# Kernel tuning notes

Hardware: AMD Instinct MI355X
Metric: run time of the kernel (lower is better)

The kernel has to match this reference:

```python
import jax, jax.numpy as jnp
import numpy as np

EPS = 1e-5
DIM, QK, PDIM, SR = 256, 64, 128, 2
B, H, W = 16, 64, 64
SCALE = QK ** (-0.5)


def _conv(x, w, stride, pad, groups=1):
    return jax.lax.conv_general_dilated(
        x, w, (stride, stride), [(pad, pad), (pad, pad)], feature_group_count=groups)


def _bn(x, g, b, m, v):
    # inference-mode BatchNorm2d with running stats
    s = (g / jnp.sqrt(v + EPS))[None, :, None, None]
    return (x - m[None, :, None, None]) * s + b[None, :, None, None]


def _gn1(x, g, b):
    # GroupNorm(1, C): normalize over (C,H,W) per sample
    mu = x.mean(axis=(1, 2, 3), keepdims=True)
    var = x.var(axis=(1, 2, 3), keepdims=True)
    xh = (x - mu) / jnp.sqrt(var + EPS)
    return xh * g[None, :, None, None] + b[None, :, None, None]


def setup_inputs() -> dict:
    key = jax.random.key(0)
    ks = jax.random.split(key, 6)
    inp = {
        'x': jax.random.normal(ks[0], (B, DIM, H, W), jnp.float32),
        'gn_g': jnp.ones((DIM,), jnp.float32),
        'gn_b': jnp.zeros((DIM,), jnp.float32),
        'w_in': jax.random.normal(ks[1], (2 * QK + DIM, DIM, 3, 3), jnp.float32) * 0.05,
        'bn_in_g': jnp.ones((2 * QK + DIM,), jnp.float32),
        'bn_in_b': jnp.zeros((2 * QK + DIM,), jnp.float32),
        'bn_in_m': jnp.zeros((2 * QK + DIM,), jnp.float32),
        'bn_in_v': jnp.ones((2 * QK + DIM,), jnp.float32),
        'w_k': jax.random.normal(ks[2], (QK, 1, SR, SR), jnp.float32) * 0.05,
        'bn_k_g': jnp.ones((QK,), jnp.float32),
        'bn_k_b': jnp.zeros((QK,), jnp.float32),
        'bn_k_m': jnp.zeros((QK,), jnp.float32),
        'bn_k_v': jnp.ones((QK,), jnp.float32),
        'w_v': jax.random.normal(ks[3], (PDIM, 1, SR, SR), jnp.float32) * 0.05,
        'bn_v_g': jnp.ones((PDIM,), jnp.float32),
        'bn_v_b': jnp.zeros((PDIM,), jnp.float32),
        'bn_v_m': jnp.zeros((PDIM,), jnp.float32),
        'bn_v_v': jnp.ones((PDIM,), jnp.float32),
        'w_out': jax.random.normal(ks[4], (DIM, DIM, 1, 1), jnp.float32) * 0.05,
        'bn_out_g': jnp.ones((DIM,), jnp.float32),
        'bn_out_b': jnp.zeros((DIM,), jnp.float32),
        'bn_out_m': jnp.zeros((DIM,), jnp.float32),
        'bn_out_v': jnp.ones((DIM,), jnp.float32),
    }
    return inp


def reference(x, gn_g, gn_b, w_in, bn_in_g, bn_in_b, bn_in_m, bn_in_v,
              w_k, bn_k_g, bn_k_b, bn_k_m, bn_k_v,
              w_v, bn_v_g, bn_v_b, bn_v_m, bn_v_v,
              w_out, bn_out_g, bn_out_b, bn_out_m, bn_out_v):
    x = _gn1(x, gn_g, gn_b)
    y = _bn(_conv(x, w_in, 1, 1), bn_in_g, bn_in_b, bn_in_m, bn_in_v)
    q = y[:, :QK]
    k = y[:, QK:2 * QK]
    v = y[:, 2 * QK:2 * QK + PDIM]
    u = y[:, 2 * QK + PDIM:]
    # depthwise sr-stride convs reduce k/v spatially
    k = _bn(_conv(k, w_k, SR, 0, groups=QK), bn_k_g, bn_k_b, bn_k_m, bn_k_v)
    v = _bn(_conv(v, w_v, SR, 0, groups=PDIM), bn_v_g, bn_v_b, bn_v_m, bn_v_v)
    b, _, h, w = u.shape
    qf = q.reshape(b, QK, -1)      # [B, QK, N]
    kf = k.reshape(b, QK, -1)      # [B, QK, M]
    vf = v.reshape(b, PDIM, -1)    # [B, PDIM, M]
    attn = jnp.einsum('bcn,bcm->bnm', qf, kf) * SCALE
    attn = jax.nn.softmax(attn, axis=-1)
    o = jnp.einsum('bcm,bnm->bcn', vf, attn).reshape(b, PDIM, h, w)
    cat = jnp.concatenate([o, u], axis=1)
    out = _bn(_conv(jax.nn.relu(cat), w_out, 1, 0), bn_out_g, bn_out_b, bn_out_m, bn_out_v)
    return out
```

## Files before the change

### kernel.cpp

```cpp
#include <hip/hip_runtime.h>
#include <stdint.h>

#define EPSV 1e-5f

typedef __attribute__((ext_vector_type(8))) short short8;
typedef __attribute__((ext_vector_type(4))) float f32x4;
typedef __bf16 bf16x8 __attribute__((ext_vector_type(8)));

__device__ __forceinline__ unsigned short f2bf(float f) {
  union { float f; unsigned int u; } v; v.f = f;
  unsigned int r = (v.u + 0x7FFFu + ((v.u >> 16) & 1u)) >> 16;
  return (unsigned short)r;
}
__device__ __forceinline__ float bf2f(unsigned short h) {
  union { unsigned int u; float f; } v; v.u = ((unsigned int)h) << 16;
  return v.f;
}

__device__ __forceinline__ f32x4 mfma16(bf16x8 a, bf16x8 b, f32x4 c) {
  return __builtin_amdgcn_mfma_f32_16x16x32_bf16(a, b, c, 0, 0, 0);
}

__device__ __forceinline__ unsigned cvt_pk_bf16(float lo, float hi) {
  unsigned r;
  asm("v_cvt_pk_bf16_f32 %0, %1, %2" : "=v"(r) : "v"(lo), "v"(hi));
  return r;
}

#define GLOAD16(g, l)                                                          \
  __builtin_amdgcn_global_load_lds(                                            \
      (const __attribute__((address_space(1))) void*)(g),                      \
      (__attribute__((address_space(3))) void*)(l), 16, 0, 0)

__global__ __launch_bounds__(256) void k_gn_stats(const float* __restrict__ x,
                                                  float* __restrict__ stats) {
  int b = blockIdx.x >> 6, chunk = blockIdx.x & 63;
  const float4* xp = (const float4*)(x + ((size_t)b << 20) + (size_t)chunk * 16384);
  int t = threadIdx.x;
  float s = 0.f, q = 0.f;
#pragma unroll
  for (int i = 0; i < 16; ++i) {
    float4 v = xp[i * 256 + t];
    s += v.x + v.y + v.z + v.w;
    q += v.x * v.x + v.y * v.y + v.z * v.z + v.w * v.w;
  }
#pragma unroll
  for (int m = 1; m <= 32; m <<= 1) { s += __shfl_xor(s, m); q += __shfl_xor(q, m); }
  __shared__ float ls[8];
  int w = t >> 6, l = t & 63;
  if (l == 0) { ls[w * 2] = s; ls[w * 2 + 1] = q; }
  __syncthreads();
  if (t == 0) {
    float S = ls[0] + ls[2] + ls[4] + ls[6];
    float Q = ls[1] + ls[3] + ls[5] + ls[7];
    atomicAdd(&stats[b * 2], S);
    atomicAdd(&stats[b * 2 + 1], Q);
  }
}

__global__ __launch_bounds__(256) void k_gn_norm(const float* __restrict__ x,
                                                 const float* __restrict__ stats,
                                                 const float* __restrict__ g,
                                                 const float* __restrict__ bb,
                                                 unsigned short* __restrict__ xnp) {
  __shared__ float tile[64][65];
  int pt = blockIdx.x;
  int ct = blockIdx.y;
  int b = blockIdx.z;
  int t = threadIdx.x, tr = t >> 6, tc = t & 63;
  const float* xb = x + ((size_t)b << 20) + (size_t)(ct * 64) * 4096 + pt * 64;
#pragma unroll
  for (int i = 0; i < 16; ++i) {
    int r = i * 4 + tr;
    tile[r][tc] = xb[(size_t)r * 4096 + tc];
  }
  __syncthreads();
  float mu = stats[b * 2] * (1.f / 1048576.f);
  float var = stats[b * 2 + 1] * (1.f / 1048576.f) - mu * mu;
  float istd = rsqrtf(var + EPSV);
  float gg = g[ct * 64 + tc] * istd;
  float bv = bb[ct * 64 + tc];
  unsigned short* out = xnp + (((size_t)b * 66 + (pt + 1)) * 66 + 1) * 256 + ct * 64 + tc;
#pragma unroll
  for (int i = 0; i < 16; ++i) {
    int pcol = i * 4 + tr;
    float v = (tile[tc][pcol] - mu) * gg + bv;
    out[(size_t)pcol * 256] = f2bf(v);
  }
}

__global__ __launch_bounds__(256) void k_prep_wt(const float* __restrict__ w_in,
                                                 const float* __restrict__ bg,
                                                 const float* __restrict__ bv,
                                                 unsigned short* __restrict__ wt) {
  int idx = blockIdx.x * 256 + threadIdx.x;
  if (idx >= 9 * 384 * 256) return;
  int tap = idx / 98304;
  int rem = idx - tap * 98304;
  int co = rem >> 8, ci = rem & 255;
  float s = bg[co] * rsqrtf(bv[co] + EPSV);
  wt[idx] = f2bf(w_in[(size_t)(co * 256 + ci) * 9 + tap] * s);
}

__global__ __launch_bounds__(256) void k_prep_misc(
    const float* w_out, const float* og, const float* ob, const float* om, const float* ov,
    const float* big, const float* bib, const float* bim, const float* biv,
    const float* w_k, const float* kg, const float* kb, const float* km, const float* kvv,
    const float* w_v, const float* vg, const float* vb, const float* vm, const float* vvv,
    unsigned short* wo2, float* bias_in, float* bias_out,
    float* wkf, float* bias_k, float* wvf, float* bias_v) {
  int idx = blockIdx.x * 256 + threadIdx.x;
  if (idx < 65536) {
    int co = idx >> 8;
    float s = og[co] * rsqrtf(ov[co] + EPSV);
    wo2[idx] = f2bf(w_out[idx] * s);
    return;
  }
  idx -= 65536;
  if (idx < 384) {
    float s = big[idx] * rsqrtf(biv[idx] + EPSV);
    bias_in[idx] = bib[idx] - bim[idx] * s;
    return;
  }
  idx -= 384;
  if (idx < 256) {
    float s = og[idx] * rsqrtf(ov[idx] + EPSV);
    bias_out[idx] = ob[idx] - om[idx] * s;
    return;
  }
  idx -= 256;
  if (idx < 64) {
    float s = kg[idx] * rsqrtf(kvv[idx] + EPSV);
#pragma unroll
    for (int tp = 0; tp < 4; ++tp) wkf[idx * 4 + tp] = w_k[idx * 4 + tp] * s;
    bias_k[idx] = kb[idx] - km[idx] * s;
    return;
  }
  idx -= 64;
  if (idx < 128) {
    float s = vg[idx] * rsqrtf(vvv[idx] + EPSV);
#pragma unroll
    for (int tp = 0; tp < 4; ++tp) wvf[idx * 4 + tp] = w_v[idx * 4 + tp] * s;
    bias_v[idx] = vb[idx] - vm[idx] * s;
    return;
  }
}

__global__ __launch_bounds__(256) void k_conv3(const unsigned short* __restrict__ xnp,
                                               const unsigned short* __restrict__ wt,
                                               const float* __restrict__ bias_in,
                                               unsigned short* __restrict__ y) {
  int pt = blockIdx.x, cot = blockIdx.y, b = blockIdx.z;
  int p0 = pt * 128, co0 = cot * 128;
  __shared__ alignas(16) unsigned short As[128 * 64];
  __shared__ alignas(16) unsigned short Bs[128 * 64];
  int t = threadIdx.x, w = t >> 6, l = t & 63;
  int rr = t >> 3, c8 = (t & 7) * 8;
  int lg = l >> 4, lr = l & 15;

  int baseA[4];
#pragma unroll
  for (int i = 0; i < 4; ++i) {
    int p = p0 + i * 32 + rr;
    int yy = p >> 6, xx = p & 63;
    baseA[i] = ((b * 66 + yy) * 66 + xx) * 256 + c8;
  }
  int baseB = (co0 + rr) * 256 + c8;

  f32x4 acc[4][4];
#pragma unroll
  for (int i = 0; i < 4; ++i)
#pragma unroll
    for (int j = 0; j < 4; ++j) acc[i][j] = f32x4{0.f, 0.f, 0.f, 0.f};

  int wr = (w >> 1) * 64, wc = (w & 1) * 64;

  for (int tap = 0; tap < 9; ++tap) {
    int aoff = ((tap / 3) * 66 + (tap % 3)) * 256;
#pragma unroll 1
    for (int kc = 0; kc < 4; ++kc) {
      int ci0 = kc * 64;
      __syncthreads();
#pragma unroll
      for (int i = 0; i < 4; ++i) {
        GLOAD16(xnp + baseA[i] + aoff + ci0, &As[(i * 32 + w * 8) * 64]);
        GLOAD16(wt + baseB + tap * 98304 + i * 8192 + ci0, &Bs[(i * 32 + w * 8) * 64]);
      }
      __syncthreads();
      bf16x8 af[4][2], bf[4][2];
#pragma unroll
      for (int mt = 0; mt < 4; ++mt)
#pragma unroll
        for (int k2 = 0; k2 < 2; ++k2) {
          af[mt][k2] = *(const bf16x8*)&As[(wr + mt * 16 + lr) * 64 + k2 * 32 + lg * 8];
          bf[mt][k2] = *(const bf16x8*)&Bs[(wc + mt * 16 + lr) * 64 + k2 * 32 + lg * 8];
        }
#pragma unroll
      for (int mt = 0; mt < 4; ++mt)
#pragma unroll
        for (int nt = 0; nt < 4; ++nt) {
          acc[mt][nt] = mfma16(af[mt][0], bf[nt][0], acc[mt][nt]);
          acc[mt][nt] = mfma16(af[mt][1], bf[nt][1], acc[mt][nt]);
        }
    }
  }
  float bias[4];
  int coBase = co0 + wc;
#pragma unroll
  for (int nt = 0; nt < 4; ++nt) bias[nt] = bias_in[coBase + nt * 16 + lr];
#pragma unroll
  for (int mt = 0; mt < 4; ++mt) {
    int p = p0 + wr + mt * 16 + lg * 4;
#pragma unroll
    for (int r = 0; r < 4; ++r) {
      size_t rowoff = ((size_t)(b * 4096 + p + r)) * 384;
#pragma unroll
      for (int nt = 0; nt < 4; ++nt) {
        int co = coBase + nt * 16 + lr;
        float v = acc[mt][nt][r] + bias[nt];
        if (co >= 256) v = fmaxf(v, 0.f);
        y[rowoff + co] = f2bf(v);
      }
    }
  }
}

__global__ __launch_bounds__(256) void k_kv(const unsigned short* __restrict__ y,
                                            const float* __restrict__ wkf, const float* __restrict__ bias_k,
                                            const float* __restrict__ wvf, const float* __restrict__ bias_v,
                                            unsigned short* __restrict__ kk, unsigned short* __restrict__ vv) {
  constexpr int LDW = 200;
  __shared__ unsigned short ty[128 * LDW];
  __shared__ unsigned short vt[128 * 33];
  int b = blockIdx.x >> 5, my = blockIdx.x & 31;
  int t = threadIdx.x;
  const unsigned short* ybase = y + ((size_t)(b * 4096 + my * 128)) * 384 + 64;
#pragma unroll
  for (int j = 0; j < 12; ++j) {
    int idx = j * 256 + t;
    int row = idx / 24, c8 = idx - row * 24;
    bf16x8 v = *(const bf16x8*)&ybase[(size_t)row * 384 + c8 * 8];
    *(bf16x8*)&ty[row * LDW + c8 * 8] = v;
  }
  __syncthreads();

  {
    int c = t & 63, wq = t >> 6;
    float wk0 = wkf[c * 4 + 0], wk1 = wkf[c * 4 + 1];
    float wk2 = wkf[c * 4 + 2], wk3 = wkf[c * 4 + 3];
    float bk = bias_k[c];
#pragma unroll
    for (int pass = 0; pass < 8; ++pass) {
      int mx = pass * 4 + wq;
      int r0 = 2 * mx, r1 = 2 * mx + 1;
      float a = bk;
      a += bf2f(ty[r0 * LDW + c]) * wk0;
      a += bf2f(ty[(r0 + 1) * LDW + c]) * wk1;
      a += bf2f(ty[(64 + r0) * LDW + c]) * wk2;
      a += bf2f(ty[(64 + r1) * LDW + c]) * wk3;
      kk[((size_t)(b * 1024 + my * 32 + mx)) * 64 + c] = f2bf(a);
    }
  }

  {
    int cv = t & 127, mxh = t >> 7;
    float wv0 = wvf[cv * 4 + 0], wv1 = wvf[cv * 4 + 1];
    float wv2 = wvf[cv * 4 + 2], wv3 = wvf[cv * 4 + 3];
    float bv = bias_v[cv];
    int col = 64 + cv;
#pragma unroll
    for (int pass = 0; pass < 16; ++pass) {
      int mx = pass * 2 + mxh;
      int r0 = 2 * mx, r1 = 2 * mx + 1;
      float a = bv;
      a += bf2f(ty[r0 * LDW + col]) * wv0;
      a += bf2f(ty[r1 * LDW + col]) * wv1;
      a += bf2f(ty[(64 + r0) * LDW + col]) * wv2;
      a += bf2f(ty[(64 + r1) * LDW + col]) * wv3;
      vt[cv * 33 + mx] = f2bf(a);
    }
  }
  __syncthreads();
  {
    int mx = t & 31, cvq = t >> 5;
#pragma unroll
    for (int i = 0; i < 16; ++i) {
      int cv = i * 8 + cvq;
      vv[((size_t)(b * 128 + cv)) * 1024 + my * 32 + mx] = vt[cv * 33 + mx];
    }
  }
}

__global__ __launch_bounds__(512, 4) void k_attn(unsigned short* __restrict__ y,
                                                 const unsigned short* __restrict__ kk,
                                                 const unsigned short* __restrict__ vvb) {
  __shared__ alignas(16) unsigned short Ks[2][4096];
  __shared__ alignas(16) unsigned short PT[8][64][16];
  int blk = blockIdx.x;
  int b = blk >> 5, ntile = blk & 31;
  int t = threadIdx.x, w = t >> 6, l = t & 63;
  int lg = l >> 4, lr = l & 15;
  int nq0 = ntile * 128 + w * 16;
  const float SC = 0.125f * 1.44269504f;

  union { short8 s; bf16x8 b; } uo;
#pragma unroll
  for (int i = 0; i < 8; ++i) uo.s[i] = (short)0x3F80;
  bf16x8 ones = uo.b;

  bf16x8 qf[2];
#pragma unroll
  for (int c = 0; c < 2; ++c)
    qf[c] = *(const bf16x8*)&y[((size_t)(b * 4096 + nq0 + lr)) * 384 + c * 32 + lg * 8];

  f32x4 oa[8];
#pragma unroll
  for (int tt = 0; tt < 8; ++tt) oa[tt] = f32x4{0.f, 0.f, 0.f, 0.f};
  float mi[4], li[4];
#pragma unroll
  for (int r = 0; r < 4; ++r) { mi[r] = -1e30f; li[r] = 0.f; }

  int srow = t >> 3;
  int skg = (t & 7) ^ (srow & 7);
  const unsigned short* ksrc = kk + ((size_t)(b * 1024 + srow)) * 64 + skg * 8;
  unsigned short* ldst0 = &Ks[0][w * 512];
  unsigned short* ldst1 = &Ks[1][w * 512];

  GLOAD16(ksrc, ldst0);
  __syncthreads();

  for (int it = 0; it < 16; ++it) {
    int cur = it & 1;
    const unsigned short* Kc = &Ks[cur][0];
    if (it < 15) GLOAD16(ksrc + (it + 1) * 4096, cur ? ldst0 : ldst1);

    f32x4 s[4];
#pragma unroll
    for (int mt = 0; mt < 4; ++mt) {
      int row = mt * 16 + lr;
      int sw = (lr & 7) << 3;
      bf16x8 kf0 = *(const bf16x8*)&Kc[row * 64 + ((lg * 8) ^ sw)];
      bf16x8 kf1 = *(const bf16x8*)&Kc[row * 64 + ((32 + lg * 8) ^ sw)];
      f32x4 z = f32x4{0.f, 0.f, 0.f, 0.f};
      z = mfma16(qf[0], kf0, z);
      z = mfma16(qf[1], kf1, z);
      s[mt] = z;
    }

    float rm[4];
#pragma unroll
    for (int r = 0; r < 4; ++r)
      rm[r] = fmaxf(fmaxf(s[0][r], s[1][r]), fmaxf(s[2][r], s[3][r]));
#pragma unroll
    for (int msk = 1; msk <= 8; msk <<= 1)
#pragma unroll
      for (int r = 0; r < 4; ++r) rm[r] = fmaxf(rm[r], __shfl_xor(rm[r], msk));
    bool grow = false;
#pragma unroll
    for (int r = 0; r < 4; ++r) grow |= (rm[r] * SC > mi[r]);
    if (__any(grow)) {
#pragma unroll
      for (int r = 0; r < 4; ++r) {
        float nm = fmaxf(mi[r], rm[r] * SC);
        float corr = exp2f(mi[r] - nm);
        mi[r] = nm;
        li[r] *= corr;
#pragma unroll
        for (int tt = 0; tt < 8; ++tt) oa[tt][r] *= corr;
      }
    }
#pragma unroll
    for (int mt = 0; mt < 4; ++mt)
#pragma unroll
      for (int r = 0; r < 4; ++r)
        s[mt][r] = exp2f(fmaf(s[mt][r], SC, -mi[r]));

#pragma unroll
    for (int mt = 0; mt < 4; ++mt) {
      unsigned p01 = cvt_pk_bf16(s[mt][0], s[mt][1]);
      unsigned p23 = cvt_pk_bf16(s[mt][2], s[mt][3]);
      unsigned long long pk = ((unsigned long long)p23 << 32) | p01;
      *(unsigned long long*)&PT[w][mt * 16 + lr][lg * 4] = pk;
    }
    asm volatile("s_waitcnt lgkmcnt(0)" ::: "memory");

    bf16x8 pf[2];
#pragma unroll
    for (int kc = 0; kc < 2; ++kc) {
      unsigned base = (unsigned)(uintptr_t)&PT[w][kc * 32 + lg * 8][lr];
      unsigned r0x, r0y, r1x, r1y;
      uint2 t0, t1;
      asm volatile("ds_read_b64_tr_b16 %0, %1" : "=v"(t0) : "v"(base));
      asm volatile("ds_read_b64_tr_b16 %0, %1 offset:128" : "=v"(t1) : "v"(base));
      union { unsigned u[4]; bf16x8 b; } cv;
      cv.u[0] = t0.x; cv.u[1] = t0.y; cv.u[2] = t1.x; cv.u[3] = t1.y;
      pf[kc] = cv.b;
      (void)r0x; (void)r0y; (void)r1x; (void)r1y;
    }
    asm volatile("s_waitcnt lgkmcnt(0)" ::: "memory");
    __builtin_amdgcn_sched_barrier(0);

    {
      f32x4 zz = f32x4{0.f, 0.f, 0.f, 0.f};
      zz = mfma16(pf[0], ones, zz);
      zz = mfma16(pf[1], ones, zz);
#pragma unroll
      for (int r = 0; r < 4; ++r) li[r] += zz[r];
    }

    size_t vbase = ((size_t)(b * 128)) * 1024 + it * 64 + lg * 8;
#pragma unroll
    for (int tt = 0; tt < 8; ++tt) {
      const unsigned short* vr = &vvb[vbase + (size_t)(tt * 16 + lr) * 1024];
      bf16x8 vf0 = *(const bf16x8*)&vr[0];
      bf16x8 vf1 = *(const bf16x8*)&vr[32];
      oa[tt] = mfma16(pf[0], vf0, oa[tt]);
      oa[tt] = mfma16(pf[1], vf1, oa[tt]);
    }
    __syncthreads();
  }

#pragma unroll
  for (int r = 0; r < 4; ++r) {
    float inv = 1.f / li[r];
    int p = nq0 + lg * 4 + r;
    size_t rowoff = ((size_t)(b * 4096 + p)) * 384 + 128;
#pragma unroll
    for (int tt = 0; tt < 8; ++tt) {
      float v = oa[tt][r] * inv;
      v = fmaxf(v, 0.f);
      y[rowoff + tt * 16 + lr] = f2bf(v);
    }
  }
}

__global__ __launch_bounds__(256) void k_conv1(const unsigned short* __restrict__ y,
                                               const unsigned short* __restrict__ wo2,
                                               const float* __restrict__ bias_out,
                                               float* __restrict__ out) {
  int ptile = blockIdx.x, cot = blockIdx.y, b = blockIdx.z;
  int p0 = ptile * 128, co0 = cot * 128;
  __shared__ alignas(16) unsigned short As[128 * 64];
  __shared__ alignas(16) unsigned short Bs[128 * 64];
  int t = threadIdx.x, w = t >> 6, l = t & 63;
  int rr = t >> 3, c8 = (t & 7) * 8;
  int lg = l >> 4, lr = l & 15;
  int baseA = (co0 + rr) * 256 + c8;
  size_t baseB = ((size_t)(b * 4096 + p0 + rr)) * 384 + 128 + c8;
  f32x4 acc[4][4];
#pragma unroll
  for (int i = 0; i < 4; ++i)
#pragma unroll
    for (int j = 0; j < 4; ++j) acc[i][j] = f32x4{0.f, 0.f, 0.f, 0.f};
  int wr = (w >> 1) * 64, wc = (w & 1) * 64;
#pragma unroll 1
  for (int kc = 0; kc < 4; ++kc) {
    int ci0 = kc * 64;
    __syncthreads();
#pragma unroll
    for (int i = 0; i < 4; ++i) {
      GLOAD16(wo2 + baseA + i * 8192 + ci0, &As[(i * 32 + w * 8) * 64]);
      GLOAD16(y + baseB + (size_t)i * 32 * 384 + ci0, &Bs[(i * 32 + w * 8) * 64]);
    }
    __syncthreads();
    bf16x8 af[4][2], bf[4][2];
#pragma unroll
    for (int mt = 0; mt < 4; ++mt)
#pragma unroll
      for (int k2 = 0; k2 < 2; ++k2) {
        af[mt][k2] = *(const bf16x8*)&As[(wr + mt * 16 + lr) * 64 + k2 * 32 + lg * 8];
        bf[mt][k2] = *(const bf16x8*)&Bs[(wc + mt * 16 + lr) * 64 + k2 * 32 + lg * 8];
      }
#pragma unroll
    for (int mt = 0; mt < 4; ++mt)
#pragma unroll
      for (int nt = 0; nt < 4; ++nt) {
        acc[mt][nt] = mfma16(af[mt][0], bf[nt][0], acc[mt][nt]);
        acc[mt][nt] = mfma16(af[mt][1], bf[nt][1], acc[mt][nt]);
      }
  }
#pragma unroll
  for (int mt = 0; mt < 4; ++mt)
#pragma unroll
    for (int r = 0; r < 4; ++r) {
      int co = co0 + wr + mt * 16 + lg * 4 + r;
      float bv = bias_out[co];
      size_t obase = ((size_t)(b * 256 + co)) << 12;
#pragma unroll
      for (int nt = 0; nt < 4; ++nt) {
        int p = p0 + wc + nt * 16 + lr;
        out[obase + p] = acc[mt][nt][r] + bv;
      }
    }
}

static constexpr size_t pad256(size_t x) { return (x + 255) & ~(size_t)255; }

extern "C" void kernel_launch(void* const* d_in, const int* in_sizes, int n_in,
                              void* d_out, int out_size, void* d_ws, size_t ws_size,
                              hipStream_t stream) {
  const float* x      = (const float*)d_in[0];
  const float* gn_g   = (const float*)d_in[1];
  const float* gn_b   = (const float*)d_in[2];
  const float* w_in   = (const float*)d_in[3];
  const float* bin_g  = (const float*)d_in[4];
  const float* bin_b  = (const float*)d_in[5];
  const float* bin_m  = (const float*)d_in[6];
  const float* bin_v  = (const float*)d_in[7];
  const float* w_k    = (const float*)d_in[8];
  const float* bk_g   = (const float*)d_in[9];
  const float* bk_b   = (const float*)d_in[10];
  const float* bk_m   = (const float*)d_in[11];
  const float* bk_v   = (const float*)d_in[12];
  const float* w_v    = (const float*)d_in[13];
  const float* bv_g   = (const float*)d_in[14];
  const float* bv_b   = (const float*)d_in[15];
  const float* bv_m   = (const float*)d_in[16];
  const float* bv_v   = (const float*)d_in[17];
  const float* w_out  = (const float*)d_in[18];
  const float* bo_g   = (const float*)d_in[19];
  const float* bo_b   = (const float*)d_in[20];
  const float* bo_m   = (const float*)d_in[21];
  const float* bo_v   = (const float*)d_in[22];
  float* out = (float*)d_out;

  char* ws = (char*)d_ws;
  size_t off = 0;
  float*          stats   = (float*)(ws + off);          off += pad256(128);
  unsigned short* wt      = (unsigned short*)(ws + off); off += pad256((size_t)9 * 384 * 256 * 2);
  float*          bias_in = (float*)(ws + off);          off += pad256(384 * 4);
  unsigned short* wo2     = (unsigned short*)(ws + off); off += pad256(256 * 256 * 2);
  float*          bias_out= (float*)(ws + off);          off += pad256(256 * 4);
  float*          wkf     = (float*)(ws + off);          off += pad256(64 * 4 * 4);
  float*          bias_k  = (float*)(ws + off);          off += pad256(64 * 4);
  float*          wvf     = (float*)(ws + off);          off += pad256(128 * 4 * 4);
  float*          bias_v  = (float*)(ws + off);          off += pad256(128 * 4);
  unsigned short* xnp     = (unsigned short*)(ws + off); off += pad256((size_t)16 * 66 * 66 * 256 * 2);
  unsigned short* y       = (unsigned short*)(ws + off); off += pad256((size_t)16 * 4096 * 384 * 2);
  unsigned short* kk      = (unsigned short*)(ws + off); off += pad256((size_t)16 * 1024 * 64 * 2);
  unsigned short* vv      = (unsigned short*)(ws + off); off += pad256((size_t)16 * 128 * 1024 * 2);
  (void)ws_size; (void)out_size; (void)n_in; (void)in_sizes;

  hipMemsetAsync(stats, 0, 256, stream);
  hipMemsetAsync(xnp, 0, (size_t)16 * 66 * 66 * 256 * 2, stream);

  k_gn_stats<<<1024, 256, 0, stream>>>(x, stats);
  k_prep_wt<<<3456, 256, 0, stream>>>(w_in, bin_g, bin_v, wt);
  k_prep_misc<<<260, 256, 0, stream>>>(w_out, bo_g, bo_b, bo_m, bo_v,
                                       bin_g, bin_b, bin_m, bin_v,
                                       w_k, bk_g, bk_b, bk_m, bk_v,
                                       w_v, bv_g, bv_b, bv_m, bv_v,
                                       wo2, bias_in, bias_out, wkf, bias_k, wvf, bias_v);
  k_gn_norm<<<dim3(64, 4, 16), 256, 0, stream>>>(x, stats, gn_g, gn_b, xnp);
  k_conv3<<<dim3(32, 3, 16), 256, 0, stream>>>(xnp, wt, bias_in, y);
  k_kv<<<512, 256, 0, stream>>>(y, wkf, bias_k, wvf, bias_v, kk, vv);
  k_attn<<<512, 512, 0, stream>>>(y, kk, vv);
  k_conv1<<<dim3(32, 2, 16), 256, 0, stream>>>(y, wo2, bias_out, out);
}
```

Measured before the change: 469.1 us.

## Double-buffer conv3 GEMM with larger 256x192 tiles and XOR-swizzled LDS

Rewrites the 3x3 implicit-GEMM conv kernel to use 512-thread blocks computing 256x192 output tiles. The global-to-LDS loads are double-buffered so the next K-step is fetched while MFMAs run on the current one. LDS rows are XOR-swizzled to avoid bank conflicts, and MFMA sections run at raised wave priority. This is meant to hide load latency and improve data reuse, at the cost of more LDS (about 112KB per block) and more accumulator registers, which may lower occupancy.

```diff
diff --git a/kernel.cpp b/kernel.cpp
--- a/kernel.cpp
+++ b/kernel.cpp
@@ -24,6 +24,13 @@
 __device__ __forceinline__ unsigned cvt_pk_bf16(float lo, float hi) {
   unsigned r;
   asm("v_cvt_pk_bf16_f32 %0, %1, %2" : "=v"(r) : "v"(lo), "v"(hi));
+  return r;
+}
+
+__device__ __forceinline__ bf16x8 dsread16(const unsigned short* p) {
+  unsigned off = (unsigned)(uintptr_t)(const __attribute__((address_space(3))) unsigned short*)p;
+  bf16x8 r;
+  asm volatile("ds_read_b128 %0, %1" : "=v"(r) : "v"(off));
   return r;
 }
 
@@ -146,78 +153,120 @@
   }
 }
 
-__global__ __launch_bounds__(256) void k_conv3(const unsigned short* __restrict__ xnp,
-                                               const unsigned short* __restrict__ wt,
-                                               const float* __restrict__ bias_in,
-                                               unsigned short* __restrict__ y) {
+__global__ __launch_bounds__(512, 2) void k_conv3(const unsigned short* __restrict__ xnp,
+                                                  const unsigned short* __restrict__ wt,
+                                                  const float* __restrict__ bias_in,
+                                                  unsigned short* __restrict__ y) {
+  __shared__ alignas(16) unsigned short As[2][256 * 64];
+  __shared__ alignas(16) unsigned short Bs[2][192 * 64];
   int pt = blockIdx.x, cot = blockIdx.y, b = blockIdx.z;
-  int p0 = pt * 128, co0 = cot * 128;
-  __shared__ alignas(16) unsigned short As[128 * 64];
-  __shared__ alignas(16) unsigned short Bs[128 * 64];
+  int p0 = pt * 256, co0 = cot * 192;
   int t = threadIdx.x, w = t >> 6, l = t & 63;
-  int rr = t >> 3, c8 = (t & 7) * 8;
   int lg = l >> 4, lr = l & 15;
-
-  int baseA[4];
+  int wrM = (w >> 2) * 128, wrN = (w & 3) * 48;
+
+  int lchunk = (t & 7) ^ ((t >> 3) & 7);
+  int abase[4];
 #pragma unroll
   for (int i = 0; i < 4; ++i) {
-    int p = p0 + i * 32 + rr;
+    int row = (i * 512 + t) >> 3;
+    int p = p0 + row;
     int yy = p >> 6, xx = p & 63;
-    baseA[i] = ((b * 66 + yy) * 66 + xx) * 256 + c8;
-  }
-  int baseB = (co0 + rr) * 256 + c8;
-
-  f32x4 acc[4][4];
-#pragma unroll
-  for (int i = 0; i < 4; ++i)
-#pragma unroll
-    for (int j = 0; j < 4; ++j) acc[i][j] = f32x4{0.f, 0.f, 0.f, 0.f};
-
-  int wr = (w >> 1) * 64, wc = (w & 1) * 64;
-
-  for (int tap = 0; tap < 9; ++tap) {
-    int aoff = ((tap / 3) * 66 + (tap % 3)) * 256;
-#pragma unroll 1
-    for (int kc = 0; kc < 4; ++kc) {
-      int ci0 = kc * 64;
-      __syncthreads();
-#pragma unroll
-      for (int i = 0; i < 4; ++i) {
-        GLOAD16(xnp + baseA[i] + aoff + ci0, &As[(i * 32 + w * 8) * 64]);
-        GLOAD16(wt + baseB + tap * 98304 + i * 8192 + ci0, &Bs[(i * 32 + w * 8) * 64]);
+    abase[i] = ((b * 66 + yy) * 66 + xx) * 256 + lchunk * 8;
+  }
+  int bbase[3];
+#pragma unroll
+  for (int i = 0; i < 3; ++i) {
+    int row = (i * 512 + t) >> 3;
+    bbase[i] = (co0 + row) * 256 + lchunk * 8;
+  }
+
+  f32x4 acc[8][3];
+#pragma unroll
+  for (int i = 0; i < 8; ++i)
+#pragma unroll
+    for (int j = 0; j < 3; ++j) acc[i][j] = f32x4{0.f, 0.f, 0.f, 0.f};
+
+#define STAGE(step, buf)                                                       \
+  do {                                                                         \
+    int tap_ = (step) >> 2, kc_ = (step) & 3;                                  \
+    int dy_ = (tap_ * 11) >> 5;                                                \
+    int dx_ = tap_ - dy_ * 3;                                                  \
+    int aoff_ = (dy_ * 66 + dx_) * 256 + kc_ * 64;                             \
+    int boff_ = tap_ * 98304 + kc_ * 64;                                       \
+    _Pragma("unroll")                                                          \
+    for (int i_ = 0; i_ < 4; ++i_)                                             \
+      GLOAD16(xnp + abase[i_] + aoff_, &As[buf][(i_ * 512 + w * 64) * 8]);     \
+    _Pragma("unroll")                                                          \
+    for (int i_ = 0; i_ < 3; ++i_)                                             \
+      GLOAD16(wt + bbase[i_] + boff_, &Bs[buf][(i_ * 512 + w * 64) * 8]);      \
+  } while (0)
+
+  STAGE(0, 0);
+
+  for (int step = 0; step < 36; ++step) {
+    int cur = step & 1;
+    asm volatile("" ::: "memory");
+    if (step < 35) {
+      STAGE(step + 1, cur ^ 1);
+      asm volatile("s_waitcnt vmcnt(7)" ::: "memory");
+    } else {
+      asm volatile("s_waitcnt vmcnt(0)" ::: "memory");
+    }
+    __builtin_amdgcn_s_barrier();
+    __builtin_amdgcn_sched_barrier(0);
+
+    const unsigned short* Ac = As[cur];
+    const unsigned short* Bc = Bs[cur];
+
+    bf16x8 bfr[2][3];
+#pragma unroll
+    for (int k2 = 0; k2 < 2; ++k2)
+#pragma unroll
+      for (int nt = 0; nt < 3; ++nt) {
+        int row = wrN + nt * 16 + lr;
+        bfr[k2][nt] = dsread16(&Bc[row * 64 + (((k2 * 4 + lg) ^ (row & 7)) * 8)]);
       }
-      __syncthreads();
-      bf16x8 af[4][2], bf[4][2];
+#pragma unroll
+    for (int mh = 0; mh < 2; ++mh) {
+      bf16x8 afr[4][2];
 #pragma unroll
       for (int mt = 0; mt < 4; ++mt)
 #pragma unroll
         for (int k2 = 0; k2 < 2; ++k2) {
-          af[mt][k2] = *(const bf16x8*)&As[(wr + mt * 16 + lr) * 64 + k2 * 32 + lg * 8];
-          bf[mt][k2] = *(const bf16x8*)&Bs[(wc + mt * 16 + lr) * 64 + k2 * 32 + lg * 8];
+          int row = wrM + mh * 64 + mt * 16 + lr;
+          afr[mt][k2] = dsread16(&Ac[row * 64 + (((k2 * 4 + lg) ^ (row & 7)) * 8)]);
         }
+      asm volatile("s_waitcnt lgkmcnt(0)" ::: "memory");
+      __builtin_amdgcn_sched_barrier(0);
+      __builtin_amdgcn_s_setprio(1);
 #pragma unroll
       for (int mt = 0; mt < 4; ++mt)
 #pragma unroll
-        for (int nt = 0; nt < 4; ++nt) {
-          acc[mt][nt] = mfma16(af[mt][0], bf[nt][0], acc[mt][nt]);
-          acc[mt][nt] = mfma16(af[mt][1], bf[nt][1], acc[mt][nt]);
+        for (int nt = 0; nt < 3; ++nt) {
+          acc[mh * 4 + mt][nt] = mfma16(afr[mt][0], bfr[0][nt], acc[mh * 4 + mt][nt]);
+          acc[mh * 4 + mt][nt] = mfma16(afr[mt][1], bfr[1][nt], acc[mh * 4 + mt][nt]);
         }
-    }
-  }
-  float bias[4];
-  int coBase = co0 + wc;
-#pragma unroll
-  for (int nt = 0; nt < 4; ++nt) bias[nt] = bias_in[coBase + nt * 16 + lr];
-#pragma unroll
-  for (int mt = 0; mt < 4; ++mt) {
-    int p = p0 + wr + mt * 16 + lg * 4;
+      __builtin_amdgcn_s_setprio(0);
+    }
+    __builtin_amdgcn_sched_barrier(0);
+    __builtin_amdgcn_s_barrier();
+  }
+#undef STAGE
+
+  float bias[3];
+#pragma unroll
+  for (int nt = 0; nt < 3; ++nt) bias[nt] = bias_in[co0 + wrN + nt * 16 + lr];
+#pragma unroll
+  for (int m8 = 0; m8 < 8; ++m8) {
 #pragma unroll
     for (int r = 0; r < 4; ++r) {
-      size_t rowoff = ((size_t)(b * 4096 + p + r)) * 384;
-#pragma unroll
-      for (int nt = 0; nt < 4; ++nt) {
-        int co = coBase + nt * 16 + lr;
-        float v = acc[mt][nt][r] + bias[nt];
+      int p = p0 + wrM + m8 * 16 + lg * 4 + r;
+      size_t rowoff = ((size_t)(b * 4096 + p)) * 384;
+#pragma unroll
+      for (int nt = 0; nt < 3; ++nt) {
+        int co = co0 + wrN + nt * 16 + lr;
+        float v = acc[m8][nt][r] + bias[nt];
         if (co >= 256) v = fmaxf(v, 0.f);
         y[rowoff + co] = f2bf(v);
       }
@@ -388,14 +437,12 @@
 #pragma unroll
     for (int kc = 0; kc < 2; ++kc) {
       unsigned base = (unsigned)(uintptr_t)&PT[w][kc * 32 + lg * 8][lr];
-      unsigned r0x, r0y, r1x, r1y;
       uint2 t0, t1;
       asm volatile("ds_read_b64_tr_b16 %0, %1" : "=v"(t0) : "v"(base));
       asm volatile("ds_read_b64_tr_b16 %0, %1 offset:128" : "=v"(t1) : "v"(base));
       union { unsigned u[4]; bf16x8 b; } cv;
       cv.u[0] = t0.x; cv.u[1] = t0.y; cv.u[2] = t1.x; cv.u[3] = t1.y;
       pf[kc] = cv.b;
-      (void)r0x; (void)r0y; (void)r1x; (void)r1y;
     }
     asm volatile("s_waitcnt lgkmcnt(0)" ::: "memory");
     __builtin_amdgcn_sched_barrier(0);
@@ -552,7 +599,7 @@
                                        w_v, bv_g, bv_b, bv_m, bv_v,
                                        wo2, bias_in, bias_out, wkf, bias_k, wvf, bias_v);
   k_gn_norm<<<dim3(64, 4, 16), 256, 0, stream>>>(x, stats, gn_g, gn_b, xnp);
-  k_conv3<<<dim3(32, 3, 16), 256, 0, stream>>>(xnp, wt, bias_in, y);
+  k_conv3<<<dim3(16, 2, 16), 512, 0, stream>>>(xnp, wt, bias_in, y);
   k_kv<<<512, 256, 0, stream>>>(y, wkf, bias_k, wvf, bias_v, kk, vv);
   k_attn<<<512, 512, 0, stream>>>(y, kk, vv);
   k_conv1<<<dim3(32, 2, 16), 256, 0, stream>>>(y, wo2, bias_out, out);
```

After: 454.1 us. 1.03x faster.
